# Kernel tuning notes

Hardware: AMD Instinct MI355X
Metric: run time of the kernel (lower is better)

## Reference

```python
import jax, jax.numpy as jnp
import numpy as np
from jax import lax

SEQ, BATCH, IN, HID = 2048, 256, 64, 128


def setup_inputs() -> dict:
    key = jax.random.key(0)
    ks = jax.random.split(key, 5)
    return {
        "x": jax.random.normal(ks[0], (SEQ, BATCH, IN), dtype=jnp.float32),
        "Wx": jax.random.normal(ks[1], (HID, IN), dtype=jnp.float32) * 0.1,
        "bx": jax.random.normal(ks[2], (HID,), dtype=jnp.float32) * 0.1,
        "Wh": jax.random.normal(ks[3], (HID, HID), dtype=jnp.float32) * 0.1,
        "bh": jax.random.normal(ks[4], (HID,), dtype=jnp.float32) * 0.1,
    }


def reference(x, Wx, bx, Wh, bh):
    # Precompute the input projection for all timesteps in one GEMM:
    # fc_x(x[t]) + bh folded in. Shape (S, B, H).
    xp = jnp.einsum("sbi,hi->sbh", x, Wx) + bx + bh

    def step(h, xt):
        # h: (B, H); fc_h(h) = h @ Wh^T (bias folded into xp)
        h_new = jnp.tanh(h @ Wh.T + xt)
        return h_new, h_new

    h0 = jnp.zeros((x.shape[1], Wh.shape[0]), dtype=x.dtype)
    _, h_seq = lax.scan(step, h0, xp)  # (S, B, H)
    return h_seq, h_seq[-1][None]  # ((S,B,H), (1,B,H))
```

## Files before the change

### kernel.cpp

```cpp
#include <hip/hip_runtime.h>

#define SEQ   2048
#define BATCH 256
#define INDIM 64
#define HID   128

struct F2 { float x, y; };

template <int CTRL>
__device__ __forceinline__ float dpp_get(float v) {
    int t = __builtin_amdgcn_update_dpp(0, __builtin_bit_cast(int, v),
                                        CTRL, 0xF, 0xF, true);
    return __builtin_bit_cast(float, t);
}

#define PK_MUL(d, a, b) asm("v_pk_mul_f32 %0, %1, %2"     : "=v"(d) : "v"(a), "v"(b))
#define PK_FMA(d, a, b) asm("v_pk_fma_f32 %0, %1, %2, %0" : "+v"(d) : "v"(a), "v"(b))

#define TANH_K (-2.885390081777927f)
__device__ __forceinline__ float tanh_pre(float d, float bias_k) {
    float m = __builtin_fmaf(d, TANH_K, bias_k);
    float e = __builtin_amdgcn_exp2f(m);
    return (1.0f - e) * __builtin_amdgcn_rcpf(1.0f + e);
}

__global__ __launch_bounds__(256)
__attribute__((amdgpu_waves_per_eu(1, 1)))
void rnn_fused(
    const float* __restrict__ x,
    const float* __restrict__ Wx,
    const float* __restrict__ bx,
    const float* __restrict__ Wh,
    const float* __restrict__ bh,
    float* __restrict__ out)
{
    const int b   = blockIdx.x;
    const int tid = threadIdx.x;
    const int l   = tid & 63;
    const int w   = tid >> 6;
    const int s   = l & 15;
    const int j0  = w * 32 + (l >> 4) * 8;

    __shared__ __align__(16) float hbuf[2][HID];

    const double* WhD = (const double*)Wh;
    const double* WxD = (const double*)Wx;
    double wA[8], wB[8], wC[8], wD[8], wX[8], wY[8];
#pragma unroll
    for (int o = 0; o < 8; ++o) {
        const int row = j0 + (o & 4) + ((o & 3) ^ (l & 3));
        const int r   = row * 64 + 2 * s;
        wA[o] = WhD[r];      wB[o] = WhD[r + 1];
        wC[o] = WhD[r + 32]; wD[o] = WhD[r + 33];
        const int rx  = row * 32 + 2 * s;
        wX[o] = WxD[rx];     wY[o] = WxD[rx + 1];
    }
    const int jj  = j0 + (l & 3);
    float bias_k  = (bx[jj]     + bh[jj])     * TANH_K;
    float bias_k2 = (bx[jj + 4] + bh[jj + 4]) * TANH_K;

    ((float*)hbuf)[tid] = 0.0f;
    __syncthreads();

    const double2* xb2 = (const double2*)(x + (size_t)b * INDIM + 4 * s);
    const size_t   S2  = (size_t)BATCH * INDIM / 4;
    double2 xa[4], xn[4];
#pragma unroll
    for (int i = 0; i < 4; ++i) xa[i] = xb2[(size_t)i * S2];

    float* outp = out + (size_t)b * HID + jj;
    const bool wr = (s < 4);
    float hv1 = 0.0f, hv2 = 0.0f;

    for (int tb = 0; tb < SEQ; tb += 4) {
        asm volatile("" : "+v"(wA[0]), "+v"(wA[1]), "+v"(wA[2]), "+v"(wA[3]),
                          "+v"(wA[4]), "+v"(wA[5]), "+v"(wA[6]), "+v"(wA[7]));
        asm volatile("" : "+v"(wB[0]), "+v"(wB[1]), "+v"(wB[2]), "+v"(wB[3]),
                          "+v"(wB[4]), "+v"(wB[5]), "+v"(wB[6]), "+v"(wB[7]));
        asm volatile("" : "+v"(wC[0]), "+v"(wC[1]), "+v"(wC[2]), "+v"(wC[3]),
                          "+v"(wC[4]), "+v"(wC[5]), "+v"(wC[6]), "+v"(wC[7]));
        asm volatile("" : "+v"(wD[0]), "+v"(wD[1]), "+v"(wD[2]), "+v"(wD[3]),
                          "+v"(wD[4]), "+v"(wD[5]), "+v"(wD[6]), "+v"(wD[7]));
        asm volatile("" : "+v"(wX[0]), "+v"(wX[1]), "+v"(wX[2]), "+v"(wX[3]),
                          "+v"(wX[4]), "+v"(wX[5]), "+v"(wX[6]), "+v"(wX[7]));
        asm volatile("" : "+v"(wY[0]), "+v"(wY[1]), "+v"(wY[2]), "+v"(wY[3]),
                          "+v"(wY[4]), "+v"(wY[5]), "+v"(wY[6]), "+v"(wY[7]));
        asm volatile("" : "+v"(bias_k), "+v"(bias_k2));

#pragma unroll
        for (int i = 0; i < 4; ++i) {
            int tp = tb + 4 + i; if (tp > SEQ - 1) tp = SEQ - 1;
            xn[i] = xb2[(size_t)tp * S2];
        }

#pragma unroll
        for (int q = 0; q < 4; ++q) {
            const double2* hbd = (const double2*)&hbuf[q & 1][0];

            const double2 H0 = hbd[s];
            const double2 H1 = hbd[16 + s];
            const double2 X  = xa[q];

            double acc[8];
#pragma unroll
            for (int o = 0; o < 8; ++o) PK_MUL(acc[o], X.x, wX[o]);
#pragma unroll
            for (int o = 0; o < 8; ++o) PK_FMA(acc[o], X.y, wY[o]);
#pragma unroll
            for (int o = 0; o < 8; ++o) PK_FMA(acc[o], H0.x, wA[o]);
#pragma unroll
            for (int o = 0; o < 8; ++o) PK_FMA(acc[o], H0.y, wB[o]);
#pragma unroll
            for (int o = 0; o < 8; ++o) PK_FMA(acc[o], H1.x, wC[o]);
#pragma unroll
            for (int o = 0; o < 8; ++o) PK_FMA(acc[o], H1.y, wD[o]);

            float a0, a1, a2, a3, a4, a5, a6, a7;
            { F2 u = __builtin_bit_cast(F2, acc[0]); a0 = u.x + u.y; }
            { F2 u = __builtin_bit_cast(F2, acc[1]); a1 = u.x + u.y; }
            { F2 u = __builtin_bit_cast(F2, acc[2]); a2 = u.x + u.y; }
            { F2 u = __builtin_bit_cast(F2, acc[3]); a3 = u.x + u.y; }
            { F2 u = __builtin_bit_cast(F2, acc[4]); a4 = u.x + u.y; }
            { F2 u = __builtin_bit_cast(F2, acc[5]); a5 = u.x + u.y; }
            { F2 u = __builtin_bit_cast(F2, acc[6]); a6 = u.x + u.y; }
            { F2 u = __builtin_bit_cast(F2, acc[7]); a7 = u.x + u.y; }

            float c0 = a0 + dpp_get<0xB1>(a1);
            float c2 = a4 + dpp_get<0xB1>(a5);
            float c1 = a2 + dpp_get<0xB1>(a3);
            float c3 = a6 + dpp_get<0xB1>(a7);
            float d1 = c0 + dpp_get<0x4E>(c1);
            float d2 = c2 + dpp_get<0x4E>(c3);
            d1 += dpp_get<0x124>(d1);
            d2 += dpp_get<0x124>(d2);
            d1 += dpp_get<0x128>(d1);
            d2 += dpp_get<0x128>(d2);

            hv1 = tanh_pre(d1, bias_k);
            hv2 = tanh_pre(d2, bias_k2);

            if (wr) {
                hbuf[(q + 1) & 1][jj]     = hv1;
                hbuf[(q + 1) & 1][jj + 4] = hv2;
                outp[0] = hv1;
                outp[4] = hv2;
            }
            outp += BATCH * HID;

            asm volatile("s_waitcnt lgkmcnt(0)" ::: "memory");
            asm volatile("s_barrier" ::: "memory");
        }

#pragma unroll
        for (int i = 0; i < 4; ++i) xa[i] = xn[i];
    }

    if (wr) {
        out[(size_t)SEQ * BATCH * HID + (size_t)b * HID + jj]     = hv1;
        out[(size_t)SEQ * BATCH * HID + (size_t)b * HID + jj + 4] = hv2;
    }
}

extern "C" void kernel_launch(void* const* d_in, const int* in_sizes, int n_in,
                              void* d_out, int out_size, void* d_ws, size_t ws_size,
                              hipStream_t stream) {
    const float* x  = (const float*)d_in[0];
    const float* Wx = (const float*)d_in[1];
    const float* bx = (const float*)d_in[2];
    const float* Wh = (const float*)d_in[3];
    const float* bh = (const float*)d_in[4];
    float* out = (float*)d_out;
    (void)in_sizes; (void)n_in; (void)d_ws; (void)ws_size; (void)out_size;
    rnn_fused<<<dim3(BATCH), dim3(256), 0, stream>>>(x, Wx, bx, Wh, bh, out);
}
```

Measured before the change: 633.1 us.

## Interleave two batch rows per block to overlap reduction with FMA chain

Each block now handles two independent batch rows with the same register-resident weights. The rows are software-pipelined so one row's reduction, tanh and store overlap with the other row's FMA chain within the same barrier interval. This is meant to hide the serial reduce-and-barrier latency of the recurrence and halve the grid to 128 blocks. The trade-off is fewer blocks (under-filling CUs), more registers, and an extra barrier phase per timestep.

```diff
diff --git a/kernel.cpp b/kernel.cpp
--- a/kernel.cpp
+++ b/kernel.cpp
@@ -34,14 +34,14 @@
     const float* __restrict__ bh,
     float* __restrict__ out)
 {
-    const int b   = blockIdx.x;
+    const int b0  = blockIdx.x * 2;
     const int tid = threadIdx.x;
     const int l   = tid & 63;
     const int w   = tid >> 6;
     const int s   = l & 15;
     const int j0  = w * 32 + (l >> 4) * 8;
 
-    __shared__ __align__(16) float hbuf[2][HID];
+    __shared__ __align__(16) float hbuf[2][2][HID];
 
     const double* WhD = (const double*)Wh;
     const double* WxD = (const double*)Wx;
@@ -59,105 +59,148 @@
     float bias_k  = (bx[jj]     + bh[jj])     * TANH_K;
     float bias_k2 = (bx[jj + 4] + bh[jj + 4]) * TANH_K;
 
-    ((float*)hbuf)[tid] = 0.0f;
+    ((float*)hbuf)[tid]       = 0.0f;
+    ((float*)hbuf)[tid + 256] = 0.0f;
     __syncthreads();
 
-    const double2* xb2 = (const double2*)(x + (size_t)b * INDIM + 4 * s);
-    const size_t   S2  = (size_t)BATCH * INDIM / 4;
-    double2 xa[4], xn[4];
-#pragma unroll
-    for (int i = 0; i < 4; ++i) xa[i] = xb2[(size_t)i * S2];
-
-    float* outp = out + (size_t)b * HID + jj;
+    const double2* xb2a = (const double2*)(x + (size_t)b0 * INDIM + 4 * s);
+    const double2* xb2b = (const double2*)(x + (size_t)(b0 + 1) * INDIM + 4 * s);
+    const size_t   S2   = (size_t)BATCH * INDIM / 4;
+
+    double2 cxA = xb2a[0],  cxB = xb2b[0];
+    double2 nxA = xb2a[S2], nxB = xb2b[S2];
+    double2 fxA, fxB;
+
+    float* outpA = out + (size_t)b0 * HID + jj;
+    float* outpB = out + (size_t)(b0 + 1) * HID + jj;
     const bool wr = (s < 4);
-    float hv1 = 0.0f, hv2 = 0.0f;
-
-    for (int tb = 0; tb < SEQ; tb += 4) {
-        asm volatile("" : "+v"(wA[0]), "+v"(wA[1]), "+v"(wA[2]), "+v"(wA[3]),
-                          "+v"(wA[4]), "+v"(wA[5]), "+v"(wA[6]), "+v"(wA[7]));
-        asm volatile("" : "+v"(wB[0]), "+v"(wB[1]), "+v"(wB[2]), "+v"(wB[3]),
-                          "+v"(wB[4]), "+v"(wB[5]), "+v"(wB[6]), "+v"(wB[7]));
-        asm volatile("" : "+v"(wC[0]), "+v"(wC[1]), "+v"(wC[2]), "+v"(wC[3]),
-                          "+v"(wC[4]), "+v"(wC[5]), "+v"(wC[6]), "+v"(wC[7]));
-        asm volatile("" : "+v"(wD[0]), "+v"(wD[1]), "+v"(wD[2]), "+v"(wD[3]),
-                          "+v"(wD[4]), "+v"(wD[5]), "+v"(wD[6]), "+v"(wD[7]));
-        asm volatile("" : "+v"(wX[0]), "+v"(wX[1]), "+v"(wX[2]), "+v"(wX[3]),
-                          "+v"(wX[4]), "+v"(wX[5]), "+v"(wX[6]), "+v"(wX[7]));
-        asm volatile("" : "+v"(wY[0]), "+v"(wY[1]), "+v"(wY[2]), "+v"(wY[3]),
-                          "+v"(wY[4]), "+v"(wY[5]), "+v"(wY[6]), "+v"(wY[7]));
-        asm volatile("" : "+v"(bias_k), "+v"(bias_k2));
-
-#pragma unroll
-        for (int i = 0; i < 4; ++i) {
-            int tp = tb + 4 + i; if (tp > SEQ - 1) tp = SEQ - 1;
-            xn[i] = xb2[(size_t)tp * S2];
-        }
-
-#pragma unroll
-        for (int q = 0; q < 4; ++q) {
-            const double2* hbd = (const double2*)&hbuf[q & 1][0];
-
-            const double2 H0 = hbd[s];
-            const double2 H1 = hbd[16 + s];
-            const double2 X  = xa[q];
-
-            double acc[8];
-#pragma unroll
-            for (int o = 0; o < 8; ++o) PK_MUL(acc[o], X.x, wX[o]);
-#pragma unroll
-            for (int o = 0; o < 8; ++o) PK_FMA(acc[o], X.y, wY[o]);
-#pragma unroll
-            for (int o = 0; o < 8; ++o) PK_FMA(acc[o], H0.x, wA[o]);
-#pragma unroll
-            for (int o = 0; o < 8; ++o) PK_FMA(acc[o], H0.y, wB[o]);
-#pragma unroll
-            for (int o = 0; o < 8; ++o) PK_FMA(acc[o], H1.x, wC[o]);
-#pragma unroll
-            for (int o = 0; o < 8; ++o) PK_FMA(acc[o], H1.y, wD[o]);
-
-            float a0, a1, a2, a3, a4, a5, a6, a7;
-            { F2 u = __builtin_bit_cast(F2, acc[0]); a0 = u.x + u.y; }
-            { F2 u = __builtin_bit_cast(F2, acc[1]); a1 = u.x + u.y; }
-            { F2 u = __builtin_bit_cast(F2, acc[2]); a2 = u.x + u.y; }
-            { F2 u = __builtin_bit_cast(F2, acc[3]); a3 = u.x + u.y; }
-            { F2 u = __builtin_bit_cast(F2, acc[4]); a4 = u.x + u.y; }
-            { F2 u = __builtin_bit_cast(F2, acc[5]); a5 = u.x + u.y; }
-            { F2 u = __builtin_bit_cast(F2, acc[6]); a6 = u.x + u.y; }
-            { F2 u = __builtin_bit_cast(F2, acc[7]); a7 = u.x + u.y; }
-
-            float c0 = a0 + dpp_get<0xB1>(a1);
-            float c2 = a4 + dpp_get<0xB1>(a5);
-            float c1 = a2 + dpp_get<0xB1>(a3);
-            float c3 = a6 + dpp_get<0xB1>(a7);
-            float d1 = c0 + dpp_get<0x4E>(c1);
-            float d2 = c2 + dpp_get<0x4E>(c3);
-            d1 += dpp_get<0x124>(d1);
-            d2 += dpp_get<0x124>(d2);
-            d1 += dpp_get<0x128>(d1);
-            d2 += dpp_get<0x128>(d2);
-
-            hv1 = tanh_pre(d1, bias_k);
-            hv2 = tanh_pre(d2, bias_k2);
-
-            if (wr) {
-                hbuf[(q + 1) & 1][jj]     = hv1;
-                hbuf[(q + 1) & 1][jj + 4] = hv2;
-                outp[0] = hv1;
-                outp[4] = hv2;
-            }
-            outp += BATCH * HID;
-
-            asm volatile("s_waitcnt lgkmcnt(0)" ::: "memory");
-            asm volatile("s_barrier" ::: "memory");
-        }
-
-#pragma unroll
-        for (int i = 0; i < 4; ++i) xa[i] = xn[i];
-    }
-
+    float hvA1 = 0.0f, hvA2 = 0.0f, hvB1 = 0.0f, hvB2 = 0.0f;
+    double accA[8], accB[8];
+
+#define PIN_WEIGHTS()                                                         \
+    asm volatile("" : "+v"(wA[0]), "+v"(wA[1]), "+v"(wA[2]), "+v"(wA[3]),      \
+                      "+v"(wA[4]), "+v"(wA[5]), "+v"(wA[6]), "+v"(wA[7]));     \
+    asm volatile("" : "+v"(wB[0]), "+v"(wB[1]), "+v"(wB[2]), "+v"(wB[3]),      \
+                      "+v"(wB[4]), "+v"(wB[5]), "+v"(wB[6]), "+v"(wB[7]));     \
+    asm volatile("" : "+v"(wC[0]), "+v"(wC[1]), "+v"(wC[2]), "+v"(wC[3]),      \
+                      "+v"(wC[4]), "+v"(wC[5]), "+v"(wC[6]), "+v"(wC[7]));     \
+    asm volatile("" : "+v"(wD[0]), "+v"(wD[1]), "+v"(wD[2]), "+v"(wD[3]),      \
+                      "+v"(wD[4]), "+v"(wD[5]), "+v"(wD[6]), "+v"(wD[7]));     \
+    asm volatile("" : "+v"(wX[0]), "+v"(wX[1]), "+v"(wX[2]), "+v"(wX[3]),      \
+                      "+v"(wX[4]), "+v"(wX[5]), "+v"(wX[6]), "+v"(wX[7]));     \
+    asm volatile("" : "+v"(wY[0]), "+v"(wY[1]), "+v"(wY[2]), "+v"(wY[3]),      \
+                      "+v"(wY[4]), "+v"(wY[5]), "+v"(wY[6]), "+v"(wY[7]));     \
+    asm volatile("" : "+v"(bias_k), "+v"(bias_k2));
+
+#define XLOAD(I)                                                              \
+    { int tp = (I) + 2; if (tp > SEQ - 1) tp = SEQ - 1;                        \
+      fxA = xb2a[(size_t)tp * S2]; fxB = xb2b[(size_t)tp * S2]; }
+
+#define XROT() { cxA = nxA; nxA = fxA; cxB = nxB; nxB = fxB; }
+
+#define FMA8(ACC, XV, H0V, H1V)                                               \
+    _Pragma("unroll") for (int o = 0; o < 8; ++o) PK_MUL(ACC[o], (XV).x, wX[o]); \
+    _Pragma("unroll") for (int o = 0; o < 8; ++o) PK_FMA(ACC[o], (XV).y, wY[o]); \
+    _Pragma("unroll") for (int o = 0; o < 8; ++o) PK_FMA(ACC[o], (H0V).x, wA[o]); \
+    _Pragma("unroll") for (int o = 0; o < 8; ++o) PK_FMA(ACC[o], (H0V).y, wB[o]); \
+    _Pragma("unroll") for (int o = 0; o < 8; ++o) PK_FMA(ACC[o], (H1V).x, wC[o]); \
+    _Pragma("unroll") for (int o = 0; o < 8; ++o) PK_FMA(ACC[o], (H1V).y, wD[o]);
+
+#define REDUCE8(ACC, HV1, HV2)                                                \
+    {                                                                         \
+        float a0, a1, a2, a3, a4, a5, a6, a7;                                 \
+        { F2 u = __builtin_bit_cast(F2, ACC[0]); a0 = u.x + u.y; }            \
+        { F2 u = __builtin_bit_cast(F2, ACC[1]); a1 = u.x + u.y; }            \
+        { F2 u = __builtin_bit_cast(F2, ACC[2]); a2 = u.x + u.y; }            \
+        { F2 u = __builtin_bit_cast(F2, ACC[3]); a3 = u.x + u.y; }            \
+        { F2 u = __builtin_bit_cast(F2, ACC[4]); a4 = u.x + u.y; }            \
+        { F2 u = __builtin_bit_cast(F2, ACC[5]); a5 = u.x + u.y; }            \
+        { F2 u = __builtin_bit_cast(F2, ACC[6]); a6 = u.x + u.y; }            \
+        { F2 u = __builtin_bit_cast(F2, ACC[7]); a7 = u.x + u.y; }            \
+        float c0 = a0 + dpp_get<0xB1>(a1);                                    \
+        float c2 = a4 + dpp_get<0xB1>(a5);                                    \
+        float c1 = a2 + dpp_get<0xB1>(a3);                                    \
+        float c3 = a6 + dpp_get<0xB1>(a7);                                    \
+        float d1 = c0 + dpp_get<0x4E>(c1);                                    \
+        float d2 = c2 + dpp_get<0x4E>(c3);                                    \
+        d1 += dpp_get<0x124>(d1);                                             \
+        d2 += dpp_get<0x124>(d2);                                             \
+        d1 += dpp_get<0x128>(d1);                                             \
+        d2 += dpp_get<0x128>(d2);                                             \
+        HV1 = tanh_pre(d1, bias_k);                                           \
+        HV2 = tanh_pre(d2, bias_k2);                                          \
+    }
+
+#define TICK1(P)                                                              \
+    {                                                                         \
+        const double2* hbd = (const double2*)&hbuf[0][P][0];                  \
+        const double2 H0 = hbd[s];                                            \
+        const double2 H1 = hbd[16 + s];                                       \
+        REDUCE8(accB, hvB1, hvB2);                                            \
+        if (wr) {                                                             \
+            hbuf[1][P][jj]     = hvB1;                                        \
+            hbuf[1][P][jj + 4] = hvB2;                                        \
+            outpB[0] = hvB1; outpB[4] = hvB2;                                 \
+        }                                                                     \
+        outpB += BATCH * HID;                                                 \
+        FMA8(accA, cxA, H0, H1);                                              \
+        asm volatile("s_waitcnt lgkmcnt(0)" ::: "memory");                    \
+        asm volatile("s_barrier" ::: "memory");                               \
+    }
+
+#define TICK2(P, Q)                                                           \
+    {                                                                         \
+        const double2* hbd = (const double2*)&hbuf[1][P][0];                  \
+        const double2 H0 = hbd[s];                                            \
+        const double2 H1 = hbd[16 + s];                                       \
+        REDUCE8(accA, hvA1, hvA2);                                            \
+        if (wr) {                                                             \
+            hbuf[0][Q][jj]     = hvA1;                                        \
+            hbuf[0][Q][jj + 4] = hvA2;                                        \
+            outpA[0] = hvA1; outpA[4] = hvA2;                                 \
+        }                                                                     \
+        outpA += BATCH * HID;                                                 \
+        FMA8(accB, cxB, H0, H1);                                              \
+        asm volatile("s_waitcnt lgkmcnt(0)" ::: "memory");                    \
+        asm volatile("s_barrier" ::: "memory");                               \
+    }
+
+    XLOAD(0);
+    {
+        const double2* hbd = (const double2*)&hbuf[0][0][0];
+        const double2 H0 = hbd[s];
+        const double2 H1 = hbd[16 + s];
+        FMA8(accA, cxA, H0, H1);
+        asm volatile("s_waitcnt lgkmcnt(0)" ::: "memory");
+        asm volatile("s_barrier" ::: "memory");
+    }
+    TICK2(0, 1);
+    XROT();
+
+    for (int m = 0; m < 1023; ++m) {
+        PIN_WEIGHTS();
+        XLOAD(2 * m + 1);
+        TICK1(1);
+        TICK2(1, 0);
+        XROT();
+        XLOAD(2 * m + 2);
+        TICK1(0);
+        TICK2(0, 1);
+        XROT();
+    }
+
+    XLOAD(2047);
+    TICK1(1);
+    TICK2(1, 0);
+
+    REDUCE8(accB, hvB1, hvB2);
     if (wr) {
-        out[(size_t)SEQ * BATCH * HID + (size_t)b * HID + jj]     = hv1;
-        out[(size_t)SEQ * BATCH * HID + (size_t)b * HID + jj + 4] = hv2;
+        outpB[0] = hvB1; outpB[4] = hvB2;
+        float* fs = out + (size_t)SEQ * BATCH * HID;
+        fs[(size_t)b0 * HID + jj]           = hvA1;
+        fs[(size_t)b0 * HID + jj + 4]       = hvA2;
+        fs[(size_t)(b0 + 1) * HID + jj]     = hvB1;
+        fs[(size_t)(b0 + 1) * HID + jj + 4] = hvB2;
     }
 }
 
@@ -171,5 +214,5 @@
     const float* bh = (const float*)d_in[4];
     float* out = (float*)d_out;
     (void)in_sizes; (void)n_in; (void)d_ws; (void)ws_size; (void)out_size;
-    rnn_fused<<<dim3(BATCH), dim3(256), 0, stream>>>(x, Wx, bx, Wh, bh, out);
-}
+    rnn_fused<<<dim3(BATCH / 2), dim3(256), 0, stream>>>(x, Wx, bx, Wh, bh, out);
+}
```

Result: slower. 1.413 ms (+123.2%).
